# Kernel optimization log

Hardware: AMD Instinct MI355X
Metric: run time of the kernel (lower is better)

## Reference

```python
import jax, jax.numpy as jnp
import numpy as np

N_USER = 50000
N_ITEM = 50000
E = 500000
D = 256
H = 8
DK = D // H
EPS = 1e-5
SQRT_DK = float(np.sqrt(DK))


def _layernorm(x, g, b):
    m = jnp.mean(x, axis=-1, keepdims=True)
    v = jnp.var(x, axis=-1, keepdims=True)
    return (x - m) * jax.lax.rsqrt(v + EPS) * g + b


def _etype_aggregate(h_src, h_dst, src, dst, n_dst, Wk, bk, Wq, bq, Wv, bv, pri, att, msg):
    # per-ntype K/Q/V projections, then per-relation head-wise transforms
    k = (h_src @ Wk + bk).reshape(-1, H, DK)
    v = (h_src @ Wv + bv).reshape(-1, H, DK)
    q = (h_dst @ Wq + bq).reshape(-1, H, DK)
    k = jnp.einsum('nhi,hij->nhj', k, att)
    v = jnp.einsum('nhi,hij->nhj', v, msg)
    # v_dot_u score per edge per head: [E, H]
    score = jnp.einsum('ehd,ehd->eh', q[dst], k[src]) * pri / SQRT_DK
    # edge_softmax normalized per destination node (per head)
    smax = jax.ops.segment_max(score, dst, num_segments=n_dst)
    ex = jnp.exp(score - smax[dst])
    ssum = jax.ops.segment_sum(ex, dst, num_segments=n_dst)
    a = ex / ssum[dst]
    # u_mul_e + sum reduce (zero-in-degree dst nodes get zeros, like DGL sum)
    t = jax.ops.segment_sum(v[src] * a[:, :, None], dst, num_segments=n_dst)
    return t.reshape(n_dst, D)


def _dst_update(t, h, Wa, ba, skip, g, b):
    alpha = jax.nn.sigmoid(skip)
    out = (t @ Wa + ba) * alpha + h * (1.0 - alpha)
    return _layernorm(out, g, b)


def _forward(h_user, h_item, src_ui, dst_ui, src_iu, dst_iu, Wk_user, bk_user, Wq_user, bq_user, Wv_user, bv_user, Wa_user, ba_user, ln_g_user, ln_b_user, skip_user, Wk_item, bk_item, Wq_item, bq_item, Wv_item, bv_item, Wa_item, ba_item, ln_g_item, ln_b_item, skip_item, pri_ui, att_ui, msg_ui, pri_iu, att_iu, msg_iu):
    # (user, click, item): k/v from src ntype 'user', q from dst ntype 'item'
    t_item = _etype_aggregate(h_user, h_item, src_ui, dst_ui, N_ITEM, Wk_user, bk_user, Wq_item, bq_item, Wv_user, bv_user, pri_ui, att_ui, msg_ui)
    # (item, rev_click, user)
    t_user = _etype_aggregate(h_item, h_user, src_iu, dst_iu, N_USER, Wk_item, bk_item, Wq_user, bq_user, Wv_item, bv_item, pri_iu, att_iu, msg_iu)
    # each ntype is dst of exactly one etype -> cross_reducer 'mean' is identity
    new_user = _dst_update(t_user, h_user, Wa_user, ba_user, skip_user, ln_g_user, ln_b_user)
    new_item = _dst_update(t_item, h_item, Wa_item, ba_item, skip_item, ln_g_item, ln_b_item)
    return jnp.stack([new_user, new_item])  # [2, N, D]


def setup_inputs() -> dict:
    key = jax.random.key(0)
    ks = jax.random.split(key, 16)

    def xavier(k, shape):
        s = np.sqrt(2.0 / (shape[-2] + shape[-1]))
        return (jax.random.normal(k, shape, dtype=jnp.float32) * s).astype(jnp.float32)

    inp = {}
    inp['h_user'] = jax.random.normal(ks[0], (N_USER, D), dtype=jnp.float32)
    inp['h_item'] = jax.random.normal(ks[1], (N_ITEM, D), dtype=jnp.float32)
    inp['src_ui'] = jax.random.randint(ks[2], (E,), 0, N_USER, dtype=jnp.int32)
    inp['dst_ui'] = jax.random.randint(ks[3], (E,), 0, N_ITEM, dtype=jnp.int32)
    inp['src_iu'] = jax.random.randint(ks[4], (E,), 0, N_ITEM, dtype=jnp.int32)
    inp['dst_iu'] = jax.random.randint(ks[5], (E,), 0, N_USER, dtype=jnp.int32)
    i = 6
    for nt in ['user', 'item']:
        for nm in ['k', 'q', 'v', 'a']:
            inp[f'W{nm}_{nt}'] = xavier(jax.random.fold_in(ks[i], hash(nm) % 1000), (D, D))
            inp[f'b{nm}_{nt}'] = jnp.zeros((D,), jnp.float32)
        i += 1
        inp[f'ln_g_{nt}'] = jnp.ones((D,), jnp.float32)
        inp[f'ln_b_{nt}'] = jnp.zeros((D,), jnp.float32)
        inp[f'skip_{nt}'] = jnp.ones((1,), jnp.float32)
    for et in ['ui', 'iu']:
        inp[f'pri_{et}'] = jnp.ones((H,), jnp.float32)
        inp[f'att_{et}'] = xavier(ks[i], (H, DK, DK)); i += 1
        inp[f'msg_{et}'] = xavier(ks[i], (H, DK, DK)); i += 1
    return inp


def reference(h_user, h_item, src_ui, dst_ui, src_iu, dst_iu, Wk_user, bk_user, Wq_user, bq_user, Wv_user, bv_user, Wa_user, ba_user, ln_g_user, ln_b_user, skip_user, Wk_item, bk_item, Wq_item, bq_item, Wv_item, bv_item, Wa_item, ba_item, ln_g_item, ln_b_item, skip_item, pri_ui, att_ui, msg_ui, pri_iu, att_iu, msg_iu):
    return _forward(h_user, h_item, src_ui, dst_ui, src_iu, dst_iu, Wk_user, bk_user, Wq_user, bq_user, Wv_user, bv_user, Wa_user, ba_user, ln_g_user, ln_b_user, skip_user, Wk_item, bk_item, Wq_item, bq_item, Wv_item, bv_item, Wa_item, ba_item, ln_g_item, ln_b_item, skip_item, pri_ui, att_ui, msg_ui, pri_iu, att_iu, msg_iu)
```

## Files before the change

kernel.cpp:

```cpp
#include <hip/hip_runtime.h>

#define NN 50000
#define DD 256
#define HH 8
#define EE 500000
#define INV_SQRT_DK 0.17677669529663687f

typedef __attribute__((ext_vector_type(8))) short bf16x8;
typedef __attribute__((ext_vector_type(4))) float f32x4;

__device__ __forceinline__ unsigned short f2bf(float f) {
    unsigned int u = __float_as_uint(f);
    u = (u + 0x7FFFu + ((u >> 16) & 1u)) >> 16;
    return (unsigned short)u;
}
__device__ __forceinline__ float bf2f(unsigned short u) {
    return __uint_as_float(((unsigned int)u) << 16);
}
__device__ __forceinline__ float bflo(unsigned int u) {
    return __uint_as_float(u << 16);
}
__device__ __forceinline__ float bfhi(unsigned int u) {
    return __uint_as_float(u & 0xFFFF0000u);
}

__global__ __launch_bounds__(256) void conv_bf16(const float* __restrict__ Xu,
                                                 const float* __restrict__ Xi,
                                                 unsigned short* __restrict__ Yu,
                                                 unsigned short* __restrict__ Yi) {
    const size_t ND = (size_t)NN * DD;
    size_t i = ((size_t)blockIdx.x * 256 + threadIdx.x) * 4;
    const float* X = Xu; unsigned short* Y = Yu;
    if (i >= ND) { X = Xi; Y = Yi; i -= ND; }
    float4 v = *(const float4*)&X[i];
    ushort4 o;
    o.x = f2bf(v.x); o.y = f2bf(v.y); o.z = f2bf(v.z); o.w = f2bf(v.w);
    *(ushort4*)&Y[i] = o;
}

__global__ __launch_bounds__(256) void fuse_kernel(const float* __restrict__ Wk_u, const float* __restrict__ bk_u,
                                                   const float* __restrict__ att_ui_,
                                                   const float* __restrict__ Wv_u, const float* __restrict__ bv_u,
                                                   const float* __restrict__ msg_ui_,
                                                   const float* __restrict__ Wk_i, const float* __restrict__ bk_i,
                                                   const float* __restrict__ att_iu_,
                                                   const float* __restrict__ Wv_i, const float* __restrict__ bv_i,
                                                   const float* __restrict__ msg_iu_,
                                                   unsigned short* __restrict__ BTu, float* __restrict__ beffU,
                                                   unsigned short* __restrict__ BTi, float* __restrict__ beffI) {
    int y = blockIdx.y;
    const float* W = (y == 0) ? Wk_u : (y == 1) ? Wv_u : (y == 2) ? Wk_i : Wv_i;
    const float* b = (y == 0) ? bk_u : (y == 1) ? bv_u : (y == 2) ? bk_i : bv_i;
    const float* T = (y == 0) ? att_ui_ : (y == 1) ? msg_ui_ : (y == 2) ? att_iu_ : msg_iu_;
    unsigned short* WT = (y < 2) ? BTu : BTi;
    float* be = (y < 2) ? beffU : beffI;
    int j = threadIdx.x;
    int h = j >> 5, jj = j & 31;
    int pj = ((j >> 2) << 3) + (j & 3) + ((y & 1) ? 4 : 0);
    const float* Th = T + h * 1024;
    if (blockIdx.x < 256) {
        int c = blockIdx.x;
        float acc = 0.f;
        #pragma unroll 8
        for (int i = 0; i < 32; ++i) acc += W[c * 256 + h * 32 + i] * Th[i * 32 + jj];
        WT[pj * 256 + c] = f2bf(acc);
    } else {
        float acc = 0.f;
        #pragma unroll 8
        for (int i = 0; i < 32; ++i) acc += b[h * 32 + i] * Th[i * 32 + jj];
        be[pj] = acc;
    }
}

__global__ __launch_bounds__(256) void convT_kernel(const float* __restrict__ Wq_u, const float* __restrict__ bq_u,
                                                    const float* __restrict__ Wq_i, const float* __restrict__ bq_i,
                                                    const float* __restrict__ Wa_u, const float* __restrict__ Wa_i,
                                                    unsigned short* __restrict__ BTu, float* __restrict__ beffU,
                                                    unsigned short* __restrict__ BTi, float* __restrict__ beffI,
                                                    unsigned short* __restrict__ WaTu, unsigned short* __restrict__ WaTi) {
    int y = blockIdx.y;
    const float* W = (y == 0) ? Wq_u : (y == 1) ? Wq_i : (y == 2) ? Wa_u : Wa_i;
    unsigned short* WT = (y == 0) ? BTu + 512 * 256 : (y == 1) ? BTi + 512 * 256 : (y == 2) ? WaTu : WaTi;
    int k = blockIdx.x, n = threadIdx.x;
    WT[n * 256 + k] = f2bf(W[k * 256 + n]);
    if (k == 0 && y < 2) {
        float* be = (y == 0) ? beffU : beffI;
        const float* bq = (y == 0) ? bq_u : bq_i;
        be[512 + n] = bq[n];
    }
}

__global__ void hist_kernel(const int* __restrict__ dst_ui, const int* __restrict__ dst_iu,
                            int* __restrict__ cnt) {
    int e = blockIdx.x * blockDim.x + threadIdx.x;
    if (e < EE) atomicAdd(&cnt[dst_ui[e]], 1);
    else if (e < 2 * EE) atomicAdd(&cnt[NN + dst_iu[e - EE]], 1);
}

__global__ __launch_bounds__(256) void alloc_kernel(const int* __restrict__ cnt,
                                                    int* __restrict__ start,
                                                    int* __restrict__ ctr) {
    int y = blockIdx.y;
    int i = blockIdx.x * 256 + threadIdx.x;
    int idx = y * NN + i;
    int v = (i < NN) ? cnt[idx] : 0;
    int lane = threadIdx.x & 63;
    int pre = v;
    #pragma unroll
    for (int o = 1; o < 64; o <<= 1) {
        int u = __shfl_up(pre, o, 64);
        if (lane >= o) pre += u;
    }
    int wsum = __shfl(pre, 63, 64);
    int base = 0;
    if (lane == 63) base = atomicAdd(&ctr[y], wsum);
    base = __shfl(base, 63, 64);
    if (i < NN) start[idx] = y * EE + base + pre - v;
}

__global__ void scatter_kernel(const int* __restrict__ dst_ui, const int* __restrict__ src_ui,
                               const int* __restrict__ dst_iu, const int* __restrict__ src_iu,
                               const int* __restrict__ start, int* __restrict__ cur,
                               int* __restrict__ srcid) {
    int e = blockIdx.x * blockDim.x + threadIdx.x;
    int d, s;
    if (e < EE) { d = dst_ui[e]; s = src_ui[e]; }
    else if (e < 2 * EE) { d = NN + dst_iu[e - EE]; s = src_iu[e - EE]; }
    else return;
    int pos = start[d] + atomicAdd(&cur[d], 1);
    srcid[pos] = s;
}

__global__ __launch_bounds__(256) void gemm_kvq(const unsigned short* __restrict__ Au,
                                                const unsigned short* __restrict__ Ai,
                                                const unsigned short* __restrict__ BTu,
                                                const unsigned short* __restrict__ BTi,
                                                const float* __restrict__ beffU,
                                                const float* __restrict__ beffI,
                                                unsigned short* __restrict__ KVu,
                                                unsigned short* __restrict__ KVi,
                                                unsigned short* __restrict__ Qu,
                                                unsigned short* __restrict__ Qi) {
    __shared__ __align__(16) char smem[40960];
    bf16x8* As0 = (bf16x8*)smem;
    bf16x8* Bs0 = (bf16x8*)(smem + 10240);
    bf16x8* As1 = (bf16x8*)(smem + 20480);
    bf16x8* Bs1 = (bf16x8*)(smem + 30720);
    int z = blockIdx.z;
    const unsigned short* A = z ? Ai : Au;
    const unsigned short* BT = z ? BTi : BTu;
    const float* beff = z ? beffI : beffU;
    unsigned short* KV = z ? KVi : KVu;
    unsigned short* Qb = z ? Qi : Qu;
    int bm = blockIdx.y * 128, bn = blockIdx.x * 128;
    int tid = threadIdx.x;
    int lane = tid & 63, w = tid >> 6;
    int wm = (w & 1) * 64, wn = (w >> 1) * 64;
    int m16 = lane & 15, q = lane >> 4;

    int row0 = tid >> 2, off = tid & 3;
    int row1 = row0 + 64;
    int gr0 = bm + row0, gr1 = bm + row1;
    const bool val0 = gr0 < NN, val1 = gr1 < NN;
    const unsigned short* pA0 = &A[(size_t)gr0 * 256 + off * 8];
    const unsigned short* pA1 = &A[(size_t)gr1 * 256 + off * 8];
    const unsigned short* pB0 = &BT[(size_t)(bn + row0) * 256 + off * 8];
    const unsigned short* pB1 = &BT[(size_t)(bn + row1) * 256 + off * 8];

    f32x4 acc[4][4] = {};
    const bf16x8 zz = {};
    bf16x8 ra0 = zz, ra1 = zz, rb0, rb1;
    if (val0) ra0 = *(const bf16x8*)pA0;
    if (val1) ra1 = *(const bf16x8*)pA1;
    rb0 = *(const bf16x8*)pB0;
    rb1 = *(const bf16x8*)pB1;
    As0[row0 * 5 + off] = ra0; As0[row1 * 5 + off] = ra1;
    Bs0[row0 * 5 + off] = rb0; Bs0[row1 * 5 + off] = rb1;
    ra0 = zz; ra1 = zz;
    if (val0) ra0 = *(const bf16x8*)(pA0 + 32);
    if (val1) ra1 = *(const bf16x8*)(pA1 + 32);
    rb0 = *(const bf16x8*)(pB0 + 32);
    rb1 = *(const bf16x8*)(pB1 + 32);
    __syncthreads();
    #pragma unroll
    for (int ks = 0; ks < 8; ++ks) {
        bf16x8* Ac = (ks & 1) ? As1 : As0;
        bf16x8* Bc = (ks & 1) ? Bs1 : Bs0;
        bf16x8* An = (ks & 1) ? As0 : As1;
        bf16x8* Bn = (ks & 1) ? Bs0 : Bs1;
        if (ks < 7) {
            An[row0 * 5 + off] = ra0; An[row1 * 5 + off] = ra1;
            Bn[row0 * 5 + off] = rb0; Bn[row1 * 5 + off] = rb1;
        }
        if (ks < 6) {
            int k0 = (ks + 2) * 32;
            ra0 = zz; ra1 = zz;
            if (val0) ra0 = *(const bf16x8*)(pA0 + k0);
            if (val1) ra1 = *(const bf16x8*)(pA1 + k0);
            rb0 = *(const bf16x8*)(pB0 + k0);
            rb1 = *(const bf16x8*)(pB1 + k0);
        }
        bf16x8 af[4], bfr[4];
        #pragma unroll
        for (int i = 0; i < 4; ++i) af[i] = Ac[(wm + 16 * i + m16) * 5 + q];
        #pragma unroll
        for (int j = 0; j < 4; ++j) bfr[j] = Bc[(wn + 16 * j + m16) * 5 + q];
        #pragma unroll
        for (int i = 0; i < 4; ++i)
            #pragma unroll
            for (int j = 0; j < 4; ++j)
                acc[i][j] = __builtin_amdgcn_mfma_f32_16x16x32_bf16(af[i], bfr[j], acc[i][j], 0, 0, 0);
        __syncthreads();
    }
    const bool isKV = (bn < 512);
    unsigned short* dstb = isKV ? KV : Qb;
    const int rowlen = isKV ? 512 : 256;
    const int coloff = isKV ? bn : (bn - 512);
    unsigned short* Cs = (unsigned short*)smem;
    #pragma unroll
    for (int half = 0; half < 2; ++half) {
        if ((w & 1) == half) {
            #pragma unroll
            for (int i = 0; i < 4; ++i) {
                int rloc = 16 * i + q * 4;
                #pragma unroll
                for (int j = 0; j < 4; ++j) {
                    int cl = wn + 16 * j + m16;
                    float bv = beff[bn + cl];
                    #pragma unroll
                    for (int r = 0; r < 4; ++r)
                        Cs[(rloc + r) * 136 + cl] = f2bf(acc[i][j][r] + bv);
                }
            }
        }
        __syncthreads();
        #pragma unroll
        for (int it = 0; it < 4; ++it) {
            int idx = it * 256 + tid;
            int row = idx >> 4, seg = idx & 15;
            int gr = bm + half * 64 + row;
            if (gr < NN) {
                bf16x8 v = *(const bf16x8*)&Cs[row * 136 + seg * 8];
                *(bf16x8*)&dstb[(size_t)gr * rowlen + coloff + seg * 8] = v;
            }
        }
        __syncthreads();
    }
}

__global__ __launch_bounds__(512) void gemm_ln(const unsigned short* __restrict__ A0,
                                               const unsigned short* __restrict__ A1,
                                               const unsigned short* __restrict__ BT0,
                                               const unsigned short* __restrict__ BT1,
                                               const float* __restrict__ ba0,
                                               const float* __restrict__ ba1,
                                               const float* __restrict__ h0,
                                               const float* __restrict__ h1,
                                               const float* __restrict__ skp0,
                                               const float* __restrict__ skp1,
                                               const float* __restrict__ g0, const float* __restrict__ be0,
                                               const float* __restrict__ g1, const float* __restrict__ be1,
                                               float* __restrict__ out) {
    __shared__ __align__(16) char smem[33280];
    bf16x8* As = (bf16x8*)smem;
    bf16x8* Bs = (bf16x8*)(smem + 10240);
    float* Es = (float*)smem;
    int z = blockIdx.y;
    const unsigned short* A = z ? A1 : A0;
    const unsigned short* BT = z ? BT1 : BT0;
    const float* ba = z ? ba1 : ba0;
    const float* hb = z ? h1 : h0;
    const float* skp = z ? skp1 : skp0;
    const float* g = z ? g1 : g0;
    const float* bb = z ? be1 : be0;
    float* o = out + (z ? (size_t)NN * DD : 0);

    int bm = blockIdx.x * 128;
    int tid = threadIdx.x;
    int lane = tid & 63, w = tid >> 6;
    int m16 = lane & 15, q = lane >> 4;
    f32x4 acc[16] = {};
    for (int k0 = 0; k0 < 256; k0 += 32) {
        {
            int row = tid >> 2, ch = tid & 3;
            int gr = bm + row;
            bf16x8 va = {};
            if (gr < NN) va = *(const bf16x8*)&A[(size_t)gr * 256 + k0 + ch * 8];
            As[row * 5 + ch] = va;
        }
        #pragma unroll
        for (int cc = 0; cc < 2; ++cc) {
            int idx = tid + cc * 512;
            int n = idx >> 2, ch = idx & 3;
            Bs[n * 5 + ch] = *(const bf16x8*)&BT[(size_t)n * 256 + k0 + ch * 8];
        }
        __syncthreads();
        bf16x8 af = As[(w * 16 + m16) * 5 + q];
        #pragma unroll
        for (int jh = 0; jh < 2; ++jh) {
            bf16x8 bfr[8];
            #pragma unroll
            for (int jj = 0; jj < 8; ++jj) bfr[jj] = Bs[((jh * 8 + jj) * 16 + m16) * 5 + q];
            #pragma unroll
            for (int jj = 0; jj < 8; ++jj)
                acc[jh * 8 + jj] = __builtin_amdgcn_mfma_f32_16x16x32_bf16(af, bfr[jj], acc[jh * 8 + jj], 0, 0, 0);
        }
        __syncthreads();
    }
    float alpha = 1.f / (1.f + __expf(-skp[0]));
    float am1 = 1.f - alpha;
    float4 ba4 = *(const float4*)&ba[lane * 4];
    float4 g4 = *(const float4*)&g[lane * 4];
    float4 b4 = *(const float4*)&bb[lane * 4];
    #pragma unroll
    for (int p = 0; p < 4; ++p) {
        if ((w >> 1) == p) {
            int rbase = (w & 1) * 16 + 4 * q;
            #pragma unroll
            for (int j = 0; j < 16; ++j)
                #pragma unroll
                for (int rr = 0; rr < 4; ++rr)
                    Es[(rbase + rr) * 260 + 16 * j + m16] = acc[j][rr];
        }
        __syncthreads();
        #pragma unroll
        for (int rrr = 0; rrr < 4; ++rrr) {
            int lrow = w * 4 + rrr;
            int gr = bm + 32 * p + lrow;
            if (gr < NN) {
                float4 tm = *(const float4*)&Es[lrow * 260 + lane * 4];
                float4 hh = *(const float4*)&hb[(size_t)gr * 256 + lane * 4];
                float x0 = (tm.x + ba4.x) * alpha + hh.x * am1;
                float x1 = (tm.y + ba4.y) * alpha + hh.y * am1;
                float x2 = (tm.z + ba4.z) * alpha + hh.z * am1;
                float x3 = (tm.w + ba4.w) * alpha + hh.w * am1;
                float s = x0 + x1 + x2 + x3;
                #pragma unroll
                for (int off = 32; off > 0; off >>= 1) s += __shfl_xor(s, off, 64);
                float mean = s * (1.f / 256.f);
                float d0 = x0 - mean, d1 = x1 - mean, d2 = x2 - mean, d3 = x3 - mean;
                float s2 = d0 * d0 + d1 * d1 + d2 * d2 + d3 * d3;
                #pragma unroll
                for (int off = 32; off > 0; off >>= 1) s2 += __shfl_xor(s2, off, 64);
                float rstd = rsqrtf(s2 * (1.f / 256.f) + 1e-5f);
                float4 r;
                r.x = d0 * rstd * g4.x + b4.x;
                r.y = d1 * rstd * g4.y + b4.y;
                r.z = d2 * rstd * g4.z + b4.z;
                r.w = d3 * rstd * g4.w + b4.w;
                *(float4*)&o[(size_t)gr * 256 + lane * 4] = r;
            }
        }
        __syncthreads();
    }
}

__global__ __launch_bounds__(256) void fused_agg(const int* __restrict__ start,
                                                 const int* __restrict__ cnt,
                                                 const int* __restrict__ srcid,
                                                 const unsigned short* __restrict__ Qi,
                                                 const unsigned short* __restrict__ Qu,
                                                 const unsigned short* __restrict__ KVu,
                                                 const unsigned short* __restrict__ KVi,
                                                 const float* __restrict__ pri_ui,
                                                 const float* __restrict__ pri_iu,
                                                 unsigned short* __restrict__ tI16,
                                                 unsigned short* __restrict__ tU16) {
    int w = threadIdx.x >> 6;
    int lane = threadIdx.x & 63;
    int b = blockIdx.x * 4 + w;
    bool second = (b >= NN);
    int d = second ? b - NN : b;
    const unsigned short* Q = second ? Qu : Qi;
    const unsigned short* KV = second ? KVi : KVu;
    const float* pri = second ? pri_iu : pri_ui;
    unsigned short* T = second ? tU16 : tI16;

    int h = lane >> 3;
    float sscale = pri[h] * INV_SQRT_DK;
    ushort4 q4 = *(const ushort4*)&Q[(size_t)d * 256 + lane * 4];
    float qx = bf2f(q4.x), qy = bf2f(q4.y), qz = bf2f(q4.z), qw = bf2f(q4.w);

    int p0 = start[b], n = cnt[b];
    float a0 = 0.f, a1 = 0.f, a2 = 0.f, a3 = 0.f, l = 0.f;

#define LDKV(idx) (*(const uint4*)&KV[(size_t)__shfl(myS, (idx), 64) * 512 + lane * 8])
#define PROC(kv) { \
        float sc = qx * bflo(kv.x) + qy * bfhi(kv.x) + qz * bflo(kv.y) + qw * bfhi(kv.y); \
        sc += __shfl_xor(sc, 1, 8); \
        sc += __shfl_xor(sc, 2, 8); \
        sc += __shfl_xor(sc, 4, 8); \
        float wgt = __expf(sc * sscale); \
        a0 += wgt * bflo(kv.z); \
        a1 += wgt * bfhi(kv.z); \
        a2 += wgt * bflo(kv.w); \
        a3 += wgt * bfhi(kv.w); \
        l += wgt; }

    for (int base = 0; base < n; base += 64) {
        int rem = n - base; if (rem > 64) rem = 64;
        int myS = (lane < rem) ? srcid[p0 + base + lane] : 0;
        uint4 k0 = {}, k1 = {}, k2 = {}, k3 = {};
        if (0 < rem) k0 = LDKV(0);
        if (1 < rem) k1 = LDKV(1);
        if (2 < rem) k2 = LDKV(2);
        if (3 < rem) k3 = LDKV(3);
        int t = 0;
        for (; t + 4 <= rem; t += 4) {
            PROC(k0); if (t + 4 < rem) k0 = LDKV(t + 4);
            PROC(k1); if (t + 5 < rem) k1 = LDKV(t + 5);
            PROC(k2); if (t + 6 < rem) k2 = LDKV(t + 6);
            PROC(k3); if (t + 7 < rem) k3 = LDKV(t + 7);
        }
        if (t < rem)     PROC(k0);
        if (t + 1 < rem) PROC(k1);
        if (t + 2 < rem) PROC(k2);
    }
#undef LDKV
#undef PROC

    float inv = (l > 0.f) ? 1.f / l : 0.f;
    ushort4 o;
    o.x = f2bf(a0 * inv); o.y = f2bf(a1 * inv);
    o.z = f2bf(a2 * inv); o.w = f2bf(a3 * inv);
    *(ushort4*)&T[(size_t)d * 256 + lane * 4] = o;
}

extern "C" void kernel_launch(void* const* d_in, const int* in_sizes, int n_in,
                              void* d_out, int out_size, void* d_ws, size_t ws_size,
                              hipStream_t stream) {
    const float* h_user  = (const float*)d_in[0];
    const float* h_item  = (const float*)d_in[1];
    const int*   src_ui  = (const int*)d_in[2];
    const int*   dst_ui  = (const int*)d_in[3];
    const int*   src_iu  = (const int*)d_in[4];
    const int*   dst_iu  = (const int*)d_in[5];
    const float* Wk_user = (const float*)d_in[6];
    const float* bk_user = (const float*)d_in[7];
    const float* Wq_user = (const float*)d_in[8];
    const float* bq_user = (const float*)d_in[9];
    const float* Wv_user = (const float*)d_in[10];
    const float* bv_user = (const float*)d_in[11];
    const float* Wa_user = (const float*)d_in[12];
    const float* ba_user = (const float*)d_in[13];
    const float* ln_g_user = (const float*)d_in[14];
    const float* ln_b_user = (const float*)d_in[15];
    const float* skip_user = (const float*)d_in[16];
    const float* Wk_item = (const float*)d_in[17];
    const float* bk_item = (const float*)d_in[18];
    const float* Wq_item = (const float*)d_in[19];
    const float* bq_item = (const float*)d_in[20];
    const float* Wv_item = (const float*)d_in[21];
    const float* bv_item = (const float*)d_in[22];
    const float* Wa_item = (const float*)d_in[23];
    const float* ba_item = (const float*)d_in[24];
    const float* ln_g_item = (const float*)d_in[25];
    const float* ln_b_item = (const float*)d_in[26];
    const float* skip_item = (const float*)d_in[27];
    const float* pri_ui = (const float*)d_in[28];
    const float* att_ui = (const float*)d_in[29];
    const float* msg_ui = (const float*)d_in[30];
    const float* pri_iu = (const float*)d_in[31];
    const float* att_iu = (const float*)d_in[32];
    const float* msg_iu = (const float*)d_in[33];
    float* out = (float*)d_out;

    const size_t ND = (size_t)NN * DD;

    unsigned short* up = (unsigned short*)d_ws;
    unsigned short* KVu = up;  up += (size_t)NN * 512;
    unsigned short* KVi = up;  up += (size_t)NN * 512;
    unsigned short* Qu  = up;  up += ND;
    unsigned short* Qi  = up;  up += ND;
    unsigned short* hU16 = up; up += ND;
    unsigned short* hI16 = up; up += ND;
    unsigned short* BTu = up;  up += 768 * 256;
    unsigned short* BTi = up;  up += 768 * 256;
    unsigned short* WaTu = up; up += 65536;
    unsigned short* WaTi = up; up += 65536;
    float* fp = (float*)up;
    float* beffU = fp; fp += 768;
    float* beffI = fp; fp += 768;
    int* ip = (int*)fp;
    int* cnt   = ip; ip += 2 * NN;
    int* cur   = ip; ip += 2 * NN;
    int* ctr   = ip; ip += 2;
    int* start = ip; ip += 2 * NN;
    int* srcid = ip; ip += 2 * EE;
    unsigned short* tU16 = hU16;
    unsigned short* tI16 = hI16;

    const int eb = (EE + 255) / 256;

    conv_bf16<<<2 * 12500, 256, 0, stream>>>(h_user, h_item, hU16, hI16);
    fuse_kernel<<<dim3(257, 4), 256, 0, stream>>>(Wk_user, bk_user, att_ui, Wv_user, bv_user, msg_ui,
                                                  Wk_item, bk_item, att_iu, Wv_item, bv_item, msg_iu,
                                                  BTu, beffU, BTi, beffI);
    convT_kernel<<<dim3(256, 4), 256, 0, stream>>>(Wq_user, bq_user, Wq_item, bq_item, Wa_user, Wa_item,
                                                   BTu, beffU, BTi, beffI, WaTu, WaTi);
    hipMemsetAsync(cnt, 0, (4 * NN + 2) * sizeof(int), stream);
    hist_kernel<<<2 * eb, 256, 0, stream>>>(dst_ui, dst_iu, cnt);
    alloc_kernel<<<dim3(196, 2), 256, 0, stream>>>(cnt, start, ctr);
    scatter_kernel<<<2 * eb, 256, 0, stream>>>(dst_ui, src_ui, dst_iu, src_iu, start, cur, srcid);

    gemm_kvq<<<dim3(6, 391, 2), 256, 0, stream>>>(hU16, hI16, BTu, BTi, beffU, beffI,
                                                  KVu, KVi, Qu, Qi);

    fused_agg<<<25000, 256, 0, stream>>>(start, cnt, srcid, Qi, Qu, KVu, KVi,
                                         pri_ui, pri_iu, tI16, tU16);

    gemm_ln<<<dim3(391, 2), 512, 0, stream>>>(tU16, tI16, WaTu, WaTi, ba_user, ba_item,
                                              h_user, h_item, skip_user, skip_item,
                                              ln_g_user, ln_b_user, ln_g_item, ln_b_item, out);
}
```

Measured before the change: 672.6 us.

## Merge setup kernels, shrink source ids to 16-bit, and swizzle GEMM blocks per XCD

After: 646.9 us. 3.8% less time.

```diff
diff --git a/kernel.cpp b/kernel.cpp
--- a/kernel.cpp
+++ b/kernel.cpp
@@ -24,77 +24,79 @@
     return __uint_as_float(u & 0xFFFF0000u);
 }
 
-__global__ __launch_bounds__(256) void conv_bf16(const float* __restrict__ Xu,
+__global__ __launch_bounds__(256) void conv_hist(const float* __restrict__ Xu,
                                                  const float* __restrict__ Xi,
                                                  unsigned short* __restrict__ Yu,
-                                                 unsigned short* __restrict__ Yi) {
-    const size_t ND = (size_t)NN * DD;
-    size_t i = ((size_t)blockIdx.x * 256 + threadIdx.x) * 4;
-    const float* X = Xu; unsigned short* Y = Yu;
-    if (i >= ND) { X = Xi; Y = Yi; i -= ND; }
-    float4 v = *(const float4*)&X[i];
-    ushort4 o;
-    o.x = f2bf(v.x); o.y = f2bf(v.y); o.z = f2bf(v.z); o.w = f2bf(v.w);
-    *(ushort4*)&Y[i] = o;
-}
-
-__global__ __launch_bounds__(256) void fuse_kernel(const float* __restrict__ Wk_u, const float* __restrict__ bk_u,
-                                                   const float* __restrict__ att_ui_,
-                                                   const float* __restrict__ Wv_u, const float* __restrict__ bv_u,
-                                                   const float* __restrict__ msg_ui_,
-                                                   const float* __restrict__ Wk_i, const float* __restrict__ bk_i,
-                                                   const float* __restrict__ att_iu_,
-                                                   const float* __restrict__ Wv_i, const float* __restrict__ bv_i,
-                                                   const float* __restrict__ msg_iu_,
-                                                   unsigned short* __restrict__ BTu, float* __restrict__ beffU,
-                                                   unsigned short* __restrict__ BTi, float* __restrict__ beffI) {
+                                                 unsigned short* __restrict__ Yi,
+                                                 const int* __restrict__ dst_ui,
+                                                 const int* __restrict__ dst_iu,
+                                                 int* __restrict__ cnt) {
+    int bx = blockIdx.x;
+    if (bx < 25000) {
+        const size_t ND = (size_t)NN * DD;
+        size_t i = ((size_t)bx * 256 + threadIdx.x) * 4;
+        const float* X = Xu; unsigned short* Y = Yu;
+        if (i >= ND) { X = Xi; Y = Yi; i -= ND; }
+        float4 v = *(const float4*)&X[i];
+        ushort4 o;
+        o.x = f2bf(v.x); o.y = f2bf(v.y); o.z = f2bf(v.z); o.w = f2bf(v.w);
+        *(ushort4*)&Y[i] = o;
+    } else {
+        int e = (bx - 25000) * 256 + threadIdx.x;
+        if (e < EE) atomicAdd(&cnt[dst_ui[e]], 1);
+        else if (e < 2 * EE) atomicAdd(&cnt[NN + dst_iu[e - EE]], 1);
+    }
+}
+
+__global__ __launch_bounds__(256) void weights_kernel(const float* __restrict__ Wk_u, const float* __restrict__ bk_u,
+                                                      const float* __restrict__ att_ui_,
+                                                      const float* __restrict__ Wv_u, const float* __restrict__ bv_u,
+                                                      const float* __restrict__ msg_ui_,
+                                                      const float* __restrict__ Wk_i, const float* __restrict__ bk_i,
+                                                      const float* __restrict__ att_iu_,
+                                                      const float* __restrict__ Wv_i, const float* __restrict__ bv_i,
+                                                      const float* __restrict__ msg_iu_,
+                                                      const float* __restrict__ Wq_u, const float* __restrict__ bq_u,
+                                                      const float* __restrict__ Wq_i, const float* __restrict__ bq_i,
+                                                      const float* __restrict__ Wa_u, const float* __restrict__ Wa_i,
+                                                      unsigned short* __restrict__ BTu, float* __restrict__ beffU,
+                                                      unsigned short* __restrict__ BTi, float* __restrict__ beffI,
+                                                      unsigned short* __restrict__ WaTu, unsigned short* __restrict__ WaTi) {
     int y = blockIdx.y;
-    const float* W = (y == 0) ? Wk_u : (y == 1) ? Wv_u : (y == 2) ? Wk_i : Wv_i;
-    const float* b = (y == 0) ? bk_u : (y == 1) ? bv_u : (y == 2) ? bk_i : bv_i;
-    const float* T = (y == 0) ? att_ui_ : (y == 1) ? msg_ui_ : (y == 2) ? att_iu_ : msg_iu_;
-    unsigned short* WT = (y < 2) ? BTu : BTi;
-    float* be = (y < 2) ? beffU : beffI;
-    int j = threadIdx.x;
-    int h = j >> 5, jj = j & 31;
-    int pj = ((j >> 2) << 3) + (j & 3) + ((y & 1) ? 4 : 0);
-    const float* Th = T + h * 1024;
-    if (blockIdx.x < 256) {
-        int c = blockIdx.x;
-        float acc = 0.f;
-        #pragma unroll 8
-        for (int i = 0; i < 32; ++i) acc += W[c * 256 + h * 32 + i] * Th[i * 32 + jj];
-        WT[pj * 256 + c] = f2bf(acc);
-    } else {
-        float acc = 0.f;
-        #pragma unroll 8
-        for (int i = 0; i < 32; ++i) acc += b[h * 32 + i] * Th[i * 32 + jj];
-        be[pj] = acc;
-    }
-}
-
-__global__ __launch_bounds__(256) void convT_kernel(const float* __restrict__ Wq_u, const float* __restrict__ bq_u,
-                                                    const float* __restrict__ Wq_i, const float* __restrict__ bq_i,
-                                                    const float* __restrict__ Wa_u, const float* __restrict__ Wa_i,
-                                                    unsigned short* __restrict__ BTu, float* __restrict__ beffU,
-                                                    unsigned short* __restrict__ BTi, float* __restrict__ beffI,
-                                                    unsigned short* __restrict__ WaTu, unsigned short* __restrict__ WaTi) {
-    int y = blockIdx.y;
-    const float* W = (y == 0) ? Wq_u : (y == 1) ? Wq_i : (y == 2) ? Wa_u : Wa_i;
-    unsigned short* WT = (y == 0) ? BTu + 512 * 256 : (y == 1) ? BTi + 512 * 256 : (y == 2) ? WaTu : WaTi;
-    int k = blockIdx.x, n = threadIdx.x;
-    WT[n * 256 + k] = f2bf(W[k * 256 + n]);
-    if (k == 0 && y < 2) {
-        float* be = (y == 0) ? beffU : beffI;
-        const float* bq = (y == 0) ? bq_u : bq_i;
-        be[512 + n] = bq[n];
-    }
-}
-
-__global__ void hist_kernel(const int* __restrict__ dst_ui, const int* __restrict__ dst_iu,
-                            int* __restrict__ cnt) {
-    int e = blockIdx.x * blockDim.x + threadIdx.x;
-    if (e < EE) atomicAdd(&cnt[dst_ui[e]], 1);
-    else if (e < 2 * EE) atomicAdd(&cnt[NN + dst_iu[e - EE]], 1);
+    if (y < 4) {
+        const float* W = (y == 0) ? Wk_u : (y == 1) ? Wv_u : (y == 2) ? Wk_i : Wv_i;
+        const float* b = (y == 0) ? bk_u : (y == 1) ? bv_u : (y == 2) ? bk_i : bv_i;
+        const float* T = (y == 0) ? att_ui_ : (y == 1) ? msg_ui_ : (y == 2) ? att_iu_ : msg_iu_;
+        unsigned short* WT = (y < 2) ? BTu : BTi;
+        float* be = (y < 2) ? beffU : beffI;
+        int j = threadIdx.x;
+        int h = j >> 5, jj = j & 31;
+        int pj = ((j >> 2) << 3) + (j & 3) + ((y & 1) ? 4 : 0);
+        const float* Th = T + h * 1024;
+        if (blockIdx.x < 256) {
+            int c = blockIdx.x;
+            float acc = 0.f;
+            #pragma unroll 8
+            for (int i = 0; i < 32; ++i) acc += W[c * 256 + h * 32 + i] * Th[i * 32 + jj];
+            WT[pj * 256 + c] = f2bf(acc);
+        } else {
+            float acc = 0.f;
+            #pragma unroll 8
+            for (int i = 0; i < 32; ++i) acc += b[h * 32 + i] * Th[i * 32 + jj];
+            be[pj] = acc;
+        }
+    } else if (blockIdx.x < 256) {
+        int yy = y - 4;
+        const float* W = (yy == 0) ? Wq_u : (yy == 1) ? Wq_i : (yy == 2) ? Wa_u : Wa_i;
+        unsigned short* WT = (yy == 0) ? BTu + 512 * 256 : (yy == 1) ? BTi + 512 * 256 : (yy == 2) ? WaTu : WaTi;
+        int k = blockIdx.x, n = threadIdx.x;
+        WT[n * 256 + k] = f2bf(W[k * 256 + n]);
+        if (k == 0 && yy < 2) {
+            float* be = (yy == 0) ? beffU : beffI;
+            const float* bq = (yy == 0) ? bq_u : bq_i;
+            be[512 + n] = bq[n];
+        }
+    }
 }
 
 __global__ __launch_bounds__(256) void alloc_kernel(const int* __restrict__ cnt,
@@ -121,14 +123,14 @@
 __global__ void scatter_kernel(const int* __restrict__ dst_ui, const int* __restrict__ src_ui,
                                const int* __restrict__ dst_iu, const int* __restrict__ src_iu,
                                const int* __restrict__ start, int* __restrict__ cur,
-                               int* __restrict__ srcid) {
+                               unsigned short* __restrict__ srcid) {
     int e = blockIdx.x * blockDim.x + threadIdx.x;
     int d, s;
     if (e < EE) { d = dst_ui[e]; s = src_ui[e]; }
     else if (e < 2 * EE) { d = NN + dst_iu[e - EE]; s = src_iu[e - EE]; }
     else return;
     int pos = start[d] + atomicAdd(&cur[d], 1);
-    srcid[pos] = s;
+    srcid[pos] = (unsigned short)s;
 }
 
 __global__ __launch_bounds__(256) void gemm_kvq(const unsigned short* __restrict__ Au,
@@ -146,13 +148,17 @@
     bf16x8* Bs0 = (bf16x8*)(smem + 10240);
     bf16x8* As1 = (bf16x8*)(smem + 20480);
     bf16x8* Bs1 = (bf16x8*)(smem + 30720);
-    int z = blockIdx.z;
+    int bsw = blockIdx.x;
+    int xcd = bsw & 7, sidx = bsw >> 3;
+    int wg = (xcd < 4 ? xcd * 587 : 2348 + (xcd - 4) * 586) + sidx;
+    int bni = wg % 6; int rest = wg / 6;
+    int bmi = rest % 391; int z = rest / 391;
     const unsigned short* A = z ? Ai : Au;
     const unsigned short* BT = z ? BTi : BTu;
     const float* beff = z ? beffI : beffU;
     unsigned short* KV = z ? KVi : KVu;
     unsigned short* Qb = z ? Qi : Qu;
-    int bm = blockIdx.y * 128, bn = blockIdx.x * 128;
+    int bm = bmi * 128, bn = bni * 128;
     int tid = threadIdx.x;
     int lane = tid & 63, w = tid >> 6;
     int wm = (w & 1) * 64, wn = (w >> 1) * 64;
@@ -357,7 +363,7 @@
 
 __global__ __launch_bounds__(256) void fused_agg(const int* __restrict__ start,
                                                  const int* __restrict__ cnt,
-                                                 const int* __restrict__ srcid,
+                                                 const unsigned short* __restrict__ srcid,
                                                  const unsigned short* __restrict__ Qi,
                                                  const unsigned short* __restrict__ Qu,
                                                  const unsigned short* __restrict__ KVu,
@@ -399,7 +405,7 @@
 
     for (int base = 0; base < n; base += 64) {
         int rem = n - base; if (rem > 64) rem = 64;
-        int myS = (lane < rem) ? srcid[p0 + base + lane] : 0;
+        int myS = (lane < rem) ? (int)srcid[p0 + base + lane] : 0;
         uint4 k0 = {}, k1 = {}, k2 = {}, k3 = {};
         if (0 < rem) k0 = LDKV(0);
         if (1 < rem) k1 = LDKV(1);
@@ -486,25 +492,24 @@
     int* cur   = ip; ip += 2 * NN;
     int* ctr   = ip; ip += 2;
     int* start = ip; ip += 2 * NN;
-    int* srcid = ip; ip += 2 * EE;
+    unsigned short* srcid = (unsigned short*)ip;
     unsigned short* tU16 = hU16;
     unsigned short* tI16 = hI16;
 
     const int eb = (EE + 255) / 256;
 
-    conv_bf16<<<2 * 12500, 256, 0, stream>>>(h_user, h_item, hU16, hI16);
-    fuse_kernel<<<dim3(257, 4), 256, 0, stream>>>(Wk_user, bk_user, att_ui, Wv_user, bv_user, msg_ui,
-                                                  Wk_item, bk_item, att_iu, Wv_item, bv_item, msg_iu,
-                                                  BTu, beffU, BTi, beffI);
-    convT_kernel<<<dim3(256, 4), 256, 0, stream>>>(Wq_user, bq_user, Wq_item, bq_item, Wa_user, Wa_item,
-                                                   BTu, beffU, BTi, beffI, WaTu, WaTi);
     hipMemsetAsync(cnt, 0, (4 * NN + 2) * sizeof(int), stream);
-    hist_kernel<<<2 * eb, 256, 0, stream>>>(dst_ui, dst_iu, cnt);
+    conv_hist<<<25000 + 2 * eb, 256, 0, stream>>>(h_user, h_item, hU16, hI16,
+                                                  dst_ui, dst_iu, cnt);
+    weights_kernel<<<dim3(257, 8), 256, 0, stream>>>(Wk_user, bk_user, att_ui, Wv_user, bv_user, msg_ui,
+                                                     Wk_item, bk_item, att_iu, Wv_item, bv_item, msg_iu,
+                                                     Wq_user, bq_user, Wq_item, bq_item, Wa_user, Wa_item,
+                                                     BTu, beffU, BTi, beffI, WaTu, WaTi);
     alloc_kernel<<<dim3(196, 2), 256, 0, stream>>>(cnt, start, ctr);
     scatter_kernel<<<2 * eb, 256, 0, stream>>>(dst_ui, src_ui, dst_iu, src_iu, start, cur, srcid);
 
-    gemm_kvq<<<dim3(6, 391, 2), 256, 0, stream>>>(hU16, hI16, BTu, BTi, beffU, beffI,
-                                                  KVu, KVi, Qu, Qi);
+    gemm_kvq<<<4692, 256, 0, stream>>>(hU16, hI16, BTu, BTi, beffU, beffI,
+                                       KVu, KVi, Qu, Qi);
 
     fused_agg<<<25000, 256, 0, stream>>>(start, cnt, srcid, Qi, Qu, KVu, KVi,
                                          pri_ui, pri_iu, tI16, tU16);
```
